# Performance work log

Hardware: AMD Instinct MI355X
Metric: run time of the kernel (lower is better)

Reference implementation:

```python
import jax, jax.numpy as jnp
import numpy as np

N_NODES = 100000
N_EDGES = 1600000
N_GRAPHS = 256
F_IN = 128
NEURON = 64
AF = 8  # attention_num_feature


def gcn_conv(h_in, W, b, src, dst, n):
    # PyG GCNConv: add self loops, symmetric normalization, XW then aggregate, + bias
    h = h_in @ W  # [N, out]
    loop = jnp.arange(n)
    s = jnp.concatenate([src, loop])
    d = jnp.concatenate([dst, loop])
    deg = jax.ops.segment_sum(jnp.ones(s.shape[0], h.dtype), d, num_segments=n)
    dis = jax.lax.rsqrt(deg)  # deg >= 1 because of self loops
    norm = dis[s] * dis[d]  # [E+N]
    msg = h[s] * norm[:, None]
    out = jax.ops.segment_sum(msg, d, num_segments=n)
    return out + b


def setup_inputs() -> dict:
    key = jax.random.key(0)
    ks = jax.random.split(key, 16)
    x = jax.random.normal(ks[0], (N_NODES, F_IN), dtype=jnp.float32)
    closeness = jax.random.normal(ks[1], (N_NODES, AF), dtype=jnp.float32)
    edge_index = jax.random.randint(ks[2], (2, N_EDGES), 0, N_NODES, dtype=jnp.int64)
    batch = jnp.sort(jax.random.randint(ks[3], (N_NODES,), 0, N_GRAPHS, dtype=jnp.int64))
    def lin(k, fi, fo):
        lim = 1.0 / np.sqrt(fi)
        return jax.random.uniform(k, (fi, fo), jnp.float32, -lim, lim)
    return {
        "x": x, "closeness": closeness,
        "W1": lin(ks[4], F_IN, NEURON), "b1": jnp.zeros((NEURON,), jnp.float32),
        "W2": lin(ks[5], NEURON, NEURON), "b2": jnp.zeros((NEURON,), jnp.float32),
        "W3": lin(ks[6], NEURON, NEURON), "b3": jnp.zeros((NEURON,), jnp.float32),
        "Wc": lin(ks[7], AF, 1), "bc": jnp.zeros((1,), jnp.float32),
        "Wa1": lin(ks[8], NEURON, 16), "ba1": jnp.zeros((16,), jnp.float32),
        "Wa2": lin(ks[9], 16, 1), "ba2": jnp.zeros((1,), jnp.float32),
        "edge_index": edge_index, "batch": batch,
    }


def reference(x, closeness, W1, b1, W2, b2, W3, b3, Wc, bc, Wa1, ba1, Wa2, ba2, edge_index, batch):
    n, G = x.shape[0], N_GRAPHS
    src, dst = edge_index[0], edge_index[1]
    h = jax.nn.relu(gcn_conv(x, W1, b1, src, dst, n))
    h = jax.nn.relu(gcn_conv(h, W2, b2, src, dst, n))
    h = jax.nn.relu(gcn_conv(h, W3, b3, src, dst, n))  # [N, 64]
    # per-graph softmax over closeness logits (vectorized form of the python loop)
    logits = (closeness @ Wc + bc)[:, 0]  # [N]
    m = jax.ops.segment_max(logits, batch, num_segments=G)
    e = jnp.exp(logits - m[batch])
    z = jax.ops.segment_sum(e, batch, num_segments=G)
    p = e / z[batch]  # softmax within each graph
    counts = jax.ops.segment_sum(jnp.ones((n,), h.dtype), batch, num_segments=G)
    counts = jnp.maximum(counts, 1.0)
    attn = p * counts[batch]  # softmax * curr_size
    # self_average: mean over nodes of attn * h  == segment_sum / count
    g = jax.ops.segment_sum(attn[:, None] * h, batch, num_segments=G) / counts[:, None]  # [G, 64]
    a = jax.nn.relu(g @ Wa1 + ba1)
    return a @ Wa2 + ba2  # [G, 1]
```

## Files before the change

### kernel.cpp

```cpp
#include <hip/hip_runtime.h>
#include <hip/hip_fp16.h>
#include <math.h>


#define BKT_SHIFT 7
#define BKT_NODES 128
#define BKT_CAP 4096
#define EPB 8192

typedef _Float16 f16x8 __attribute__((ext_vector_type(8)));
typedef float f32x4 __attribute__((ext_vector_type(4)));

__global__ __launch_bounds__(1024) void block_hist_kernel(
    const int* __restrict__ dst, int* __restrict__ hist, int E, int NBKT, int NBLK) {
  __shared__ int lh[1024];
  const int t = threadIdx.x;
  const int blk = blockIdx.x;
  for (int k = t; k < NBKT; k += 1024) lh[k] = 0;
  __syncthreads();
  const int e0 = blk * EPB;
  const int e1 = min(e0 + EPB, E);
  for (int e = e0 + t; e < e1; e += 1024) atomicAdd(&lh[dst[e] >> BKT_SHIFT], 1);
  __syncthreads();
  for (int k = t; k < NBKT; k += 1024) hist[k * NBLK + blk] = lh[k];
}

__global__ __launch_bounds__(256) void row_scan_kernel(
    const int* __restrict__ hist, int* __restrict__ ebase, int* __restrict__ btot,
    int NBLK) {
  __shared__ int sh[256];
  const int k = blockIdx.x;
  const int t = threadIdx.x;
  int v = (t < NBLK) ? hist[(long)k * NBLK + t] : 0;
  sh[t] = v;
  __syncthreads();
  for (int s = 1; s < 256; s <<= 1) {
    int add = (t >= s) ? sh[t - s] : 0;
    __syncthreads();
    sh[t] += add;
    __syncthreads();
  }
  if (t < NBLK) ebase[(long)k * NBLK + t] = sh[t] - v;
  if (t == 255) btot[k] = sh[255];
}

__global__ __launch_bounds__(1024) void bucket_scan_kernel(
    const int* __restrict__ btot, int* __restrict__ bbase, int E, int NBKT) {
  __shared__ int sh[1024];
  const int t = threadIdx.x;
  int v = (t < NBKT) ? btot[t] : 0;
  sh[t] = v;
  __syncthreads();
  for (int s = 1; s < 1024; s <<= 1) {
    int add = (t >= s) ? sh[t - s] : 0;
    __syncthreads();
    sh[t] += add;
    __syncthreads();
  }
  if (t < NBKT) bbase[t] = sh[t] - v;
  if (t == 0) bbase[NBKT] = E;
}

__global__ __launch_bounds__(1024) void group_kernel(
    const int* __restrict__ src, const int* __restrict__ dst,
    const int* __restrict__ bbase, const int* __restrict__ ebase,
    unsigned int* __restrict__ grouped, int E, int NBKT, int NBLK) {
  __shared__ int lcur[1024];
  const int t = threadIdx.x;
  const int blk = blockIdx.x;
  for (int k = t; k < NBKT; k += 1024)
    lcur[k] = bbase[k] + ebase[(long)k * NBLK + blk];
  __syncthreads();
  const int e0 = blk * EPB;
  const int e1 = min(e0 + EPB, E);
  for (int e = e0 + t; e < e1; e += 1024) {
    int d = dst[e];
    int b = d >> BKT_SHIFT;
    int pos = atomicAdd(&lcur[b], 1);
    grouped[pos] = ((unsigned int)(d & (BKT_NODES - 1)) << 17) | (unsigned int)src[e];
  }
}

__global__ __launch_bounds__(256) void bucket_build_kernel(
    const unsigned int* __restrict__ grouped, const int* __restrict__ bbase,
    int* __restrict__ csr_src, int* __restrict__ ends, float* __restrict__ dis, int N) {
  __shared__ int lcnt[BKT_NODES];
  __shared__ int lsum[BKT_NODES];
  __shared__ int lcur[BKT_NODES];
  __shared__ int stage[BKT_CAP];
  const int b = blockIdx.x;
  const int t = threadIdx.x;
  const int node0 = b << BKT_SHIFT;
  const int nn = min(BKT_NODES, N - node0);
  const int base = bbase[b];
  const int m = bbase[b + 1] - base;

  if (t < BKT_NODES) lcnt[t] = 0;
  __syncthreads();
  for (int i = t; i < m; i += 256) atomicAdd(&lcnt[grouped[base + i] >> 17], 1);
  __syncthreads();
  if (t < BKT_NODES) lsum[t] = lcnt[t];
  __syncthreads();
  for (int s = 1; s < BKT_NODES; s <<= 1) {
    int add = 0;
    if (t < BKT_NODES && t >= s) add = lsum[t - s];
    __syncthreads();
    if (t < BKT_NODES) lsum[t] += add;
    __syncthreads();
  }
  if (t < nn) {
    ends[node0 + t] = base + lsum[t];
    dis[node0 + t] = 1.0f / sqrtf((float)(lcnt[t] + 1));
    lcur[t] = lsum[t] - lcnt[t];
  }
  __syncthreads();
  if (m <= BKT_CAP) {
    for (int i = t; i < m; i += 256) {
      unsigned int v = grouped[base + i];
      int p = atomicAdd(&lcur[v >> 17], 1);
      stage[p] = (int)(v & 0x1FFFFu);
    }
    __syncthreads();
    for (int i = t; i < m; i += 256) csr_src[base + i] = stage[i];
  } else {
    for (int i = t; i < m; i += 256) {
      unsigned int v = grouped[base + i];
      int p = atomicAdd(&lcur[v >> 17], 1);
      csr_src[base + p] = (int)(v & 0x1FFFFu);
    }
  }
}


template <int K, typename Tin>
__global__ __launch_bounds__(256) void gemm_mfma_kernel(
    const Tin* __restrict__ H, const float* __restrict__ W,
    const float* __restrict__ dis, __half* __restrict__ C, int N) {
  __shared__ __align__(16) __half Hs[64 * K];
  __shared__ __align__(16) __half Ws[64 * K];
  const int t = threadIdx.x;
  const int rowBase = blockIdx.x * 64;

  if constexpr (sizeof(Tin) == 4) {
    const int NF4 = 64 * K / 4;
#pragma unroll
    for (int i = 0; i < NF4 / 256; ++i) {
      int f = t + i * 256;
      int row = f / (K / 4);
      int c4 = f % (K / 4);
      int gr = rowBase + row;
      float4 v = make_float4(0.f, 0.f, 0.f, 0.f);
      if (gr < N) v = *reinterpret_cast<const float4*>(H + (long)gr * K + c4 * 4);
      union { uint2 u; __half2 h[2]; } pk;
      pk.h[0] = __floats2half2_rn(v.x, v.y);
      pk.h[1] = __floats2half2_rn(v.z, v.w);
      int byte = (row * K + c4 * 4) * 2;
      byte ^= (row & 7) << 4;
      *reinterpret_cast<uint2*>(reinterpret_cast<char*>(Hs) + byte) = pk.u;
    }
  } else {
    const int NC = 64 * K / 8;
#pragma unroll
    for (int i = 0; i < NC / 256; ++i) {
      int f = t + i * 256;
      int row = f / (K / 8);
      int c8 = f % (K / 8);
      int gr = rowBase + row;
      uint4 v = make_uint4(0u, 0u, 0u, 0u);
      if (gr < N) v = *reinterpret_cast<const uint4*>(H + (long)gr * K + c8 * 8);
      int byte = (row * K + c8 * 8) * 2;
      byte ^= (row & 7) << 4;
      *reinterpret_cast<uint4*>(reinterpret_cast<char*>(Hs) + byte) = v;
    }
  }

  {
    const int NU = (K / 2) * 16;
#pragma unroll
    for (int i = 0; i < NU / 256; ++i) {
      int u = t + i * 256;
      int kp = u >> 4;
      int cq = u & 15;
      const float4 w0 = *reinterpret_cast<const float4*>(W + (long)(2 * kp) * 64 + cq * 4);
      const float4 w1 = *reinterpret_cast<const float4*>(W + (long)(2 * kp + 1) * 64 + cq * 4);
#pragma unroll
      for (int j = 0; j < 4; ++j) {
        int c = cq * 4 + j;
        __half2 p = __floats2half2_rn((&w0.x)[j], (&w1.x)[j]);
        int byte = (c * K + 2 * kp) * 2;
        byte ^= (c & 7) << 4;
        *reinterpret_cast<__half2*>(reinterpret_cast<char*>(Ws) + byte) = p;
      }
    }
  }
  __syncthreads();

  const int w = t >> 6;
  const int l = t & 63;
  const int r = l & 15;
  const int g = l >> 4;
  const int rowL = 16 * w + r;
  f32x4 acc[4] = {{0.f, 0.f, 0.f, 0.f}, {0.f, 0.f, 0.f, 0.f},
                  {0.f, 0.f, 0.f, 0.f}, {0.f, 0.f, 0.f, 0.f}};
#pragma unroll
  for (int s = 0; s < K / 32; ++s) {
    int abyte = (rowL * K + s * 32 + g * 8) * 2;
    abyte ^= (rowL & 7) << 4;
    f16x8 afrag = *reinterpret_cast<const f16x8*>(reinterpret_cast<const char*>(Hs) + abyte);
#pragma unroll
    for (int n = 0; n < 4; ++n) {
      int col = n * 16 + r;
      int bbyte = (col * K + s * 32 + g * 8) * 2;
      bbyte ^= (col & 7) << 4;
      f16x8 bfrag = *reinterpret_cast<const f16x8*>(reinterpret_cast<const char*>(Ws) + bbyte);
      acc[n] = __builtin_amdgcn_mfma_f32_16x16x32_f16(afrag, bfrag, acc[n], 0, 0, 0);
    }
  }

  const int outRow0 = rowBase + 16 * w + 4 * g;
#pragma unroll
  for (int j = 0; j < 4; ++j) {
    int row = outRow0 + j;
    if (row < N) {
      float dv = dis[row];
#pragma unroll
      for (int n = 0; n < 4; ++n) {
        C[(long)row * 64 + n * 16 + r] = __float2half(acc[n][j] * dv);
      }
    }
  }
}


__device__ __forceinline__ float4 h4_to_f4(uint2 u) {
  const __half2 lo = *reinterpret_cast<const __half2*>(&u.x);
  const __half2 hi = *reinterpret_cast<const __half2*>(&u.y);
  const float2 flo = __half22float2(lo);
  const float2 fhi = __half22float2(hi);
  return make_float4(flo.x, flo.y, fhi.x, fhi.y);
}

__global__ __launch_bounds__(256) void aggregate_kernel(
    const __half* __restrict__ Ts, const int* __restrict__ csr_src,
    const int* __restrict__ ends, const float* __restrict__ dis,
    const float* __restrict__ bias, __half* __restrict__ O, int N) {
  const int wid = (blockIdx.x * 256 + threadIdx.x) >> 6;
  const int l = threadIdx.x & 63;
  const int g = l >> 4;
  const int c = l & 15;
  const int d0 = wid * 4 + g;
  const bool valid = d0 < N;
  const int d = valid ? d0 : (N - 1);
  const int beg = valid ? ((d0 == 0) ? 0 : ends[d0 - 1]) : 0;
  const int m = valid ? (ends[d0] - beg) : 0;
  const uint2* Tv = (const uint2*)Ts;

  float4 a = h4_to_f4(Tv[(long)d * 16 + c]);

  int mmax = m;
  mmax = max(mmax, __shfl_xor(mmax, 16, 64));
  mmax = max(mmax, __shfl_xor(mmax, 32, 64));

  const int gbase = l & 48;

  int idx0 = (c < m) ? csr_src[beg + c] : 0;
  int idx1 = (16 + c < m) ? csr_src[beg + 16 + c] : 0;

  uint2 fr0[16], fr1[16];
  const bool has0 = (mmax > 0), has1 = (mmax > 16);
  if (has0) {
#pragma unroll
    for (int j = 0; j < 16; ++j) {
      int s = __shfl(idx0, gbase + j, 64);
      s = (j < m) ? s : d;
      fr0[j] = Tv[(long)s * 16 + c];
    }
  }
  if (has1) {
#pragma unroll
    for (int j = 0; j < 16; ++j) {
      int s = __shfl(idx1, gbase + j, 64);
      s = (j + 16 < m) ? s : d;
      fr1[j] = Tv[(long)s * 16 + c];
    }
  }
  if (has0) {
#pragma unroll
    for (int j = 0; j < 16; ++j) {
      if (j < m) {
        float4 f = h4_to_f4(fr0[j]);
        a.x += f.x; a.y += f.y; a.z += f.z; a.w += f.w;
      }
    }
  }
  if (has1) {
#pragma unroll
    for (int j = 0; j < 16; ++j) {
      if (j + 16 < m) {
        float4 f = h4_to_f4(fr1[j]);
        a.x += f.x; a.y += f.y; a.z += f.z; a.w += f.w;
      }
    }
  }

  for (int base = 32; base < mmax; base += 16) {
    const int take = m - base;
    int idx = (base + c < m) ? csr_src[beg + base + c] : 0;
    uint2 fr[16];
#pragma unroll
    for (int j = 0; j < 16; ++j) {
      int s = __shfl(idx, gbase + j, 64);
      s = (j < take) ? s : d;
      fr[j] = Tv[(long)s * 16 + c];
    }
#pragma unroll
    for (int j = 0; j < 16; ++j) {
      if (j < take) {
        float4 f = h4_to_f4(fr[j]);
        a.x += f.x; a.y += f.y; a.z += f.z; a.w += f.w;
      }
    }
  }

  if (valid) {
    const float dd = dis[d0];
    const float4 b4 = ((const float4*)bias)[c];
    union { uint2 uu; __half2 h[2]; } pk;
    pk.h[0] = __floats2half2_rn(fmaxf(a.x * dd + b4.x, 0.f),
                                fmaxf(a.y * dd + b4.y, 0.f));
    pk.h[1] = __floats2half2_rn(fmaxf(a.z * dd + b4.z, 0.f),
                                fmaxf(a.w * dd + b4.w, 0.f));
    ((uint2*)O)[(long)d0 * 16 + c] = pk.uu;
  }
}


__global__ void logits_kernel(const float* __restrict__ clo, const float* __restrict__ Wc,
                              const float* __restrict__ bc, float* __restrict__ lb, int N) {
  int i = blockIdx.x * blockDim.x + threadIdx.x;
  if (i >= N) return;
  float s = bc[0];
#pragma unroll
  for (int k = 0; k < 8; ++k) s += clo[(long)i * 8 + k] * Wc[k];
  lb[i] = s;
}

__global__ __launch_bounds__(256) void pool_kernel(
    const __half* __restrict__ h3, const float* __restrict__ lb,
    const int* __restrict__ batch, const float* __restrict__ Wa1,
    const float* __restrict__ ba1, const float* __restrict__ Wa2,
    const float* __restrict__ ba2, float* __restrict__ out, int N) {
  __shared__ int sLo, sHi;
  __shared__ float red[256];
  __shared__ float Vs[4][64];
  __shared__ float sse[4];
  __shared__ float gv[64];
  __shared__ float am[16];
  const int g = blockIdx.x;
  const int t = threadIdx.x;
  if (t == 0) {
    int lo = 0, hi = N;
    while (lo < hi) { int mid = (lo + hi) >> 1; if (batch[mid] < g) lo = mid + 1; else hi = mid; }
    sLo = lo;
    lo = 0; hi = N;
    while (lo < hi) { int mid = (lo + hi) >> 1; if (batch[mid] < g + 1) lo = mid + 1; else hi = mid; }
    sHi = lo;
  }
  __syncthreads();
  const int lo = sLo, hi = sHi;

  float lm = -1e30f;
  for (int i = lo + t; i < hi; i += 256) lm = fmaxf(lm, lb[i]);
  red[t] = lm;
  __syncthreads();
  for (int s = 128; s > 0; s >>= 1) {
    if (t < s) red[t] = fmaxf(red[t], red[t + s]);
    __syncthreads();
  }
  const float m = red[0];

  const int f = t & 63, sub = t >> 6;
  float vacc = 0.f, seacc = 0.f;
  for (int i = lo + sub; i < hi; i += 4) {
    float e = expf(lb[i] - m);
    seacc += e;
    vacc += e * __half2float(h3[(long)i * 64 + f]);
  }
  Vs[sub][f] = vacc;
  if (f == 0) sse[sub] = seacc;
  __syncthreads();
  if (t < 64) {
    float se = sse[0] + sse[1] + sse[2] + sse[3];
    float v = Vs[0][f] + Vs[1][f] + Vs[2][f] + Vs[3][f];
    gv[f] = (se > 0.f) ? v / se : 0.f;
  }
  __syncthreads();
  if (t < 16) {
    float a = ba1[t];
#pragma unroll
    for (int k2 = 0; k2 < 64; ++k2) a += gv[k2] * Wa1[k2 * 16 + t];
    am[t] = a > 0.f ? a : 0.f;
  }
  __syncthreads();
  if (t == 0) {
    float o = ba2[0];
#pragma unroll
    for (int j = 0; j < 16; ++j) o += am[j] * Wa2[j];
    out[g] = o;
  }
}


extern "C" void kernel_launch(void* const* d_in, const int* in_sizes, int n_in,
                              void* d_out, int out_size, void* d_ws, size_t ws_size,
                              hipStream_t stream) {
  const float* x   = (const float*)d_in[0];
  const float* clo = (const float*)d_in[1];
  const float* W1  = (const float*)d_in[2];
  const float* b1  = (const float*)d_in[3];
  const float* W2  = (const float*)d_in[4];
  const float* b2  = (const float*)d_in[5];
  const float* W3  = (const float*)d_in[6];
  const float* b3  = (const float*)d_in[7];
  const float* Wc  = (const float*)d_in[8];
  const float* bc  = (const float*)d_in[9];
  const float* Wa1 = (const float*)d_in[10];
  const float* ba1 = (const float*)d_in[11];
  const float* Wa2 = (const float*)d_in[12];
  const float* ba2 = (const float*)d_in[13];
  const int* edge  = (const int*)d_in[14];
  const int* batch = (const int*)d_in[15];
  float* out = (float*)d_out;

  const int N = in_sizes[15];
  const int E = in_sizes[14] / 2;
  const int G = out_size;
  const int NBKT = (N + BKT_NODES - 1) >> BKT_SHIFT;
  const int NBLK = (E + EPB - 1) / EPB;

  const int* src = edge;
  const int* dst = edge + E;

  char* p = (char*)d_ws;
  auto alloc = [&](size_t bytes) -> char* {
    char* r = p;
    p += (bytes + 255) & ~(size_t)255;
    return r;
  };
  __half* tsbuf         = (__half*)alloc((size_t)N * 64 * sizeof(__half));
  __half* bufH          = (__half*)alloc((size_t)N * 64 * sizeof(__half));
  int*   csr_src        = (int*)  alloc((size_t)E * sizeof(int));
  unsigned int* grouped = (unsigned int*)alloc((size_t)E * sizeof(unsigned int));
  int*   hist           = (int*)  alloc((size_t)NBKT * NBLK * sizeof(int));
  int*   ebase          = (int*)  alloc((size_t)NBKT * NBLK * sizeof(int));
  int*   btot           = (int*)  alloc((size_t)NBKT * sizeof(int));
  int*   bbase          = (int*)  alloc((size_t)(NBKT + 1) * sizeof(int));
  int*   ends           = (int*)  alloc((size_t)N * sizeof(int));
  float* dis            = (float*)alloc((size_t)N * sizeof(float));
  float* lb             = (float*)alloc((size_t)N * sizeof(float));
  (void)ws_size; (void)n_in;

  block_hist_kernel<<<NBLK, 1024, 0, stream>>>(dst, hist, E, NBKT, NBLK);
  row_scan_kernel<<<NBKT, 256, 0, stream>>>(hist, ebase, btot, NBLK);
  bucket_scan_kernel<<<1, 1024, 0, stream>>>(btot, bbase, E, NBKT);
  group_kernel<<<NBLK, 1024, 0, stream>>>(src, dst, bbase, ebase, grouped, E, NBKT, NBLK);
  bucket_build_kernel<<<NBKT, 256, 0, stream>>>(grouped, bbase, csr_src, ends, dis, N);

  const int gN = (N + 255) / 256;
  const int gGemm = (N + 63) / 64;
  const int gAgg  = (N + 15) / 16;

  gemm_mfma_kernel<128, float><<<gGemm, 256, 0, stream>>>(x, W1, dis, tsbuf, N);
  aggregate_kernel<<<gAgg, 256, 0, stream>>>(tsbuf, csr_src, ends, dis, b1, bufH, N);
  gemm_mfma_kernel<64, __half><<<gGemm, 256, 0, stream>>>(bufH, W2, dis, tsbuf, N);
  aggregate_kernel<<<gAgg, 256, 0, stream>>>(tsbuf, csr_src, ends, dis, b2, bufH, N);
  gemm_mfma_kernel<64, __half><<<gGemm, 256, 0, stream>>>(bufH, W3, dis, tsbuf, N);
  aggregate_kernel<<<gAgg, 256, 0, stream>>>(tsbuf, csr_src, ends, dis, b3, bufH, N);

  logits_kernel<<<gN, 256, 0, stream>>>(clo, Wc, bc, lb, N);
  pool_kernel<<<G, 256, 0, stream>>>(bufH, lb, batch, Wa1, ba1, Wa2, ba2, out, N);
}
```

Before: 324.9 us.

## Fuse logits into pooling, compute degrees in histogram pass, shrink edges per block

Removes the separate logits kernel by computing closeness logits inline in the pooling kernel, reading closeness twice with vector loads. Node degrees are now counted with global atomics during the histogram pass, so the bucket build kernel no longer re-counts them with shared atomics. This costs an extra memset and global atomic traffic. The edges-per-block constant is also reduced, which launches more histogram and group blocks.

```diff
diff --git a/kernel.cpp b/kernel.cpp
--- a/kernel.cpp
+++ b/kernel.cpp
@@ -6,13 +6,14 @@
 #define BKT_SHIFT 7
 #define BKT_NODES 128
 #define BKT_CAP 4096
-#define EPB 8192
+#define EPB 6272
 
 typedef _Float16 f16x8 __attribute__((ext_vector_type(8)));
 typedef float f32x4 __attribute__((ext_vector_type(4)));
 
 __global__ __launch_bounds__(1024) void block_hist_kernel(
-    const int* __restrict__ dst, int* __restrict__ hist, int E, int NBKT, int NBLK) {
+    const int* __restrict__ dst, int* __restrict__ hist, int* __restrict__ deg,
+    int E, int NBKT, int NBLK) {
   __shared__ int lh[1024];
   const int t = threadIdx.x;
   const int blk = blockIdx.x;
@@ -20,7 +21,11 @@
   __syncthreads();
   const int e0 = blk * EPB;
   const int e1 = min(e0 + EPB, E);
-  for (int e = e0 + t; e < e1; e += 1024) atomicAdd(&lh[dst[e] >> BKT_SHIFT], 1);
+  for (int e = e0 + t; e < e1; e += 1024) {
+    int d = dst[e];
+    atomicAdd(&lh[d >> BKT_SHIFT], 1);
+    atomicAdd(&deg[d], 1);
+  }
   __syncthreads();
   for (int k = t; k < NBKT; k += 1024) hist[k * NBLK + blk] = lh[k];
 }
@@ -83,7 +88,8 @@
 
 __global__ __launch_bounds__(256) void bucket_build_kernel(
     const unsigned int* __restrict__ grouped, const int* __restrict__ bbase,
-    int* __restrict__ csr_src, int* __restrict__ ends, float* __restrict__ dis, int N) {
+    const int* __restrict__ deg, int* __restrict__ csr_src,
+    int* __restrict__ ends, float* __restrict__ dis, int N) {
   __shared__ int lcnt[BKT_NODES];
   __shared__ int lsum[BKT_NODES];
   __shared__ int lcur[BKT_NODES];
@@ -95,11 +101,11 @@
   const int base = bbase[b];
   const int m = bbase[b + 1] - base;
 
-  if (t < BKT_NODES) lcnt[t] = 0;
-  __syncthreads();
-  for (int i = t; i < m; i += 256) atomicAdd(&lcnt[grouped[base + i] >> 17], 1);
-  __syncthreads();
-  if (t < BKT_NODES) lsum[t] = lcnt[t];
+  if (t < BKT_NODES) {
+    int cnt = (t < nn) ? deg[node0 + t] : 0;
+    lcnt[t] = cnt;
+    lsum[t] = cnt;
+  }
   __syncthreads();
   for (int s = 1; s < BKT_NODES; s <<= 1) {
     int add = 0;
@@ -335,18 +341,9 @@
 }
 
 
-__global__ void logits_kernel(const float* __restrict__ clo, const float* __restrict__ Wc,
-                              const float* __restrict__ bc, float* __restrict__ lb, int N) {
-  int i = blockIdx.x * blockDim.x + threadIdx.x;
-  if (i >= N) return;
-  float s = bc[0];
-#pragma unroll
-  for (int k = 0; k < 8; ++k) s += clo[(long)i * 8 + k] * Wc[k];
-  lb[i] = s;
-}
-
 __global__ __launch_bounds__(256) void pool_kernel(
-    const __half* __restrict__ h3, const float* __restrict__ lb,
+    const __half* __restrict__ h3, const float* __restrict__ clo,
+    const float* __restrict__ Wc, const float* __restrict__ bc,
     const int* __restrict__ batch, const float* __restrict__ Wa1,
     const float* __restrict__ ba1, const float* __restrict__ Wa2,
     const float* __restrict__ ba2, float* __restrict__ out, int N) {
@@ -369,8 +366,19 @@
   __syncthreads();
   const int lo = sLo, hi = sHi;
 
+  float wc[8];
+#pragma unroll
+  for (int k = 0; k < 8; ++k) wc[k] = Wc[k];
+  const float bc0 = bc[0];
+
   float lm = -1e30f;
-  for (int i = lo + t; i < hi; i += 256) lm = fmaxf(lm, lb[i]);
+  for (int i = lo + t; i < hi; i += 256) {
+    const float4 c0 = *reinterpret_cast<const float4*>(clo + (long)i * 8);
+    const float4 c1 = *reinterpret_cast<const float4*>(clo + (long)i * 8 + 4);
+    float s = bc0 + c0.x * wc[0] + c0.y * wc[1] + c0.z * wc[2] + c0.w * wc[3]
+                  + c1.x * wc[4] + c1.y * wc[5] + c1.z * wc[6] + c1.w * wc[7];
+    lm = fmaxf(lm, s);
+  }
   red[t] = lm;
   __syncthreads();
   for (int s = 128; s > 0; s >>= 1) {
@@ -382,7 +390,11 @@
   const int f = t & 63, sub = t >> 6;
   float vacc = 0.f, seacc = 0.f;
   for (int i = lo + sub; i < hi; i += 4) {
-    float e = expf(lb[i] - m);
+    const float4 c0 = *reinterpret_cast<const float4*>(clo + (long)i * 8);
+    const float4 c1 = *reinterpret_cast<const float4*>(clo + (long)i * 8 + 4);
+    float s = bc0 + c0.x * wc[0] + c0.y * wc[1] + c0.z * wc[2] + c0.w * wc[3]
+                  + c1.x * wc[4] + c1.y * wc[5] + c1.z * wc[6] + c1.w * wc[7];
+    float e = expf(s - m);
     seacc += e;
     vacc += e * __half2float(h3[(long)i * 64 + f]);
   }
@@ -456,17 +468,17 @@
   int*   btot           = (int*)  alloc((size_t)NBKT * sizeof(int));
   int*   bbase          = (int*)  alloc((size_t)(NBKT + 1) * sizeof(int));
   int*   ends           = (int*)  alloc((size_t)N * sizeof(int));
+  int*   deg            = (int*)  alloc((size_t)N * sizeof(int));
   float* dis            = (float*)alloc((size_t)N * sizeof(float));
-  float* lb             = (float*)alloc((size_t)N * sizeof(float));
   (void)ws_size; (void)n_in;
 
-  block_hist_kernel<<<NBLK, 1024, 0, stream>>>(dst, hist, E, NBKT, NBLK);
+  hipMemsetAsync(deg, 0, (size_t)N * sizeof(int), stream);
+  block_hist_kernel<<<NBLK, 1024, 0, stream>>>(dst, hist, deg, E, NBKT, NBLK);
   row_scan_kernel<<<NBKT, 256, 0, stream>>>(hist, ebase, btot, NBLK);
   bucket_scan_kernel<<<1, 1024, 0, stream>>>(btot, bbase, E, NBKT);
   group_kernel<<<NBLK, 1024, 0, stream>>>(src, dst, bbase, ebase, grouped, E, NBKT, NBLK);
-  bucket_build_kernel<<<NBKT, 256, 0, stream>>>(grouped, bbase, csr_src, ends, dis, N);
-
-  const int gN = (N + 255) / 256;
+  bucket_build_kernel<<<NBKT, 256, 0, stream>>>(grouped, bbase, deg, csr_src, ends, dis, N);
+
   const int gGemm = (N + 63) / 64;
   const int gAgg  = (N + 15) / 16;
 
@@ -477,6 +489,5 @@
   gemm_mfma_kernel<64, __half><<<gGemm, 256, 0, stream>>>(bufH, W3, dis, tsbuf, N);
   aggregate_kernel<<<gAgg, 256, 0, stream>>>(tsbuf, csr_src, ends, dis, b3, bufH, N);
 
-  logits_kernel<<<gN, 256, 0, stream>>>(clo, Wc, bc, lb, N);
-  pool_kernel<<<G, 256, 0, stream>>>(bufH, lb, batch, Wa1, ba1, Wa2, ba2, out, N);
-}
+  pool_kernel<<<G, 256, 0, stream>>>(bufH, clo, Wc, bc, batch, Wa1, ba1, Wa2, ba2, out, N);
+}
```

After: 388.0 us. +19.4%, slower.
